# Kernel optimization log

Measured on AMD Instinct MI355X. Metric: run time of the kernel, lower is better.

Reference implementation:

```python
import jax, jax.numpy as jnp
import numpy as np

B, C, H, W = 8, 256, 128, 128
J = 8          # number of segmentation classes / fc_mu layers
S = 256        # style_length
EPS = 1e-5


def _conv3x3(x, w, b):
    # x: [B,S,H,W], w: [C,S,3,3] (OIHW), padding=1 -> SAME
    y = jax.lax.conv_general_dilated(
        x, w, window_strides=(1, 1), padding='SAME',
        dimension_numbers=('NCHW', 'OIHW', 'NCHW'))
    return y + b[None, :, None, None]


def setup_inputs() -> dict:
    key = jax.random.key(0)
    ks = jax.random.split(key, 12)
    fp = jax.random.normal(ks[0], (B, C, H, W), dtype=jnp.float32)
    # one-hot segmentation map (nearest-interpolated seg maps are one-hot)
    labels = jax.random.randint(ks[1], (B, H, W), 0, J)
    sg = jnp.transpose(jax.nn.one_hot(labels, J, dtype=jnp.float32), (0, 3, 1, 2))
    style_codes = jax.random.normal(ks[2], (B, J + 1, S), dtype=jnp.float32)
    mask_codes = jax.random.randint(ks[3], (B, J), 0, 2).astype(jnp.int32)
    # parameters
    bn_weight = jnp.ones((C,), jnp.float32)
    bn_bias = jnp.zeros((C,), jnp.float32)
    conv_gamma_w = jax.random.normal(ks[4], (C, S, 3, 3), jnp.float32) * 0.02
    conv_gamma_b = jnp.zeros((C,), jnp.float32)
    conv_beta_w = jax.random.normal(ks[5], (C, S, 3, 3), jnp.float32) * 0.02
    conv_beta_b = jnp.zeros((C,), jnp.float32)
    fc_w = jax.random.normal(ks[6], (J, S, S), jnp.float32) * 0.02  # [j, out, in]
    fc_b = jnp.zeros((J, S), jnp.float32)
    return dict(fp=fp, sg=sg, style_codes=style_codes, mask_codes=mask_codes,
                bn_weight=bn_weight, bn_bias=bn_bias,
                conv_gamma_w=conv_gamma_w, conv_gamma_b=conv_gamma_b,
                conv_beta_w=conv_beta_w, conv_beta_b=conv_beta_b,
                fc_w=fc_w, fc_b=fc_b)


def reference(fp, sg, style_codes, mask_codes, bn_weight, bn_bias,
              conv_gamma_w, conv_gamma_b, conv_beta_w, conv_beta_b,
              fc_w, fc_b):
    # BatchNorm2d (training-mode batch statistics, affine)
    mean = jnp.mean(fp, axis=(0, 2, 3), keepdims=True)
    var = jnp.var(fp, axis=(0, 2, 3), keepdims=True)
    xn = (fp - mean) * jax.lax.rsqrt(var + EPS)
    xn = xn * bn_weight[None, :, None, None] + bn_bias[None, :, None, None]

    nJ = sg.shape[1]
    # style code selection: j if mask_codes[b,j]==1 else nJ (the extra/shared code)
    idx = jnp.where(mask_codes == 1, jnp.arange(nJ)[None, :], nJ)        # [B,J]
    codes = jnp.take_along_axis(style_codes, idx[:, :, None], axis=1)    # [B,J,S]
    # per-region Linear (weights differ per region j) + ReLU
    mu = jax.nn.relu(jnp.einsum('bjs,jts->bjt', codes, fc_w) + fc_b[None])  # [B,J,S]
    # masked scatter of per-region style vectors (sg is one-hot -> exact)
    middle = jnp.einsum('bjhw,bjs->bshw', sg, mu)                         # [B,S,H,W]

    gamma = _conv3x3(middle, conv_gamma_w, conv_gamma_b)
    beta = _conv3x3(middle, conv_beta_w, conv_beta_b)
    return xn * (1.0 + gamma) + beta
```

## Files before the change

### kernel.cpp

```cpp
#include <hip/hip_runtime.h>
#include <hip/hip_fp16.h>
#include <stdint.h>

#define NB 8
#define NC 256
#define NH 128
#define NW 128
#define NJ 8
#define NS 256
#define NHW (NH*NW)
#define BN_EPS 1e-5f
#define TSTRIDE 68

__device__ inline __half2 u2h(uint32_t u) {
    union { uint32_t u; __half2 h; } x; x.u = u; return x.h;
}
__device__ inline uint32_t h2u(__half2 h) {
    union { uint32_t u; __half2 h; } x; x.h = h; return x.u;
}

__global__ __launch_bounds__(256) void kA(
        const float* __restrict__ fp, float* __restrict__ psum, float* __restrict__ psq,
        const float* __restrict__ sg, uint8_t* __restrict__ lab,
        const float* __restrict__ style, const int* __restrict__ mask,
        const float* __restrict__ fcw, const float* __restrict__ fcb,
        float* __restrict__ mu,
        const float* __restrict__ wg, const float* __restrict__ wb,
        float* __restrict__ wgt, float* __restrict__ wbt) {
    __shared__ float ls[4], lq[4];
    __shared__ float code[NS];
    __shared__ float tile[32][65];
    int blk = blockIdx.x;
    int t = threadIdx.x;
    if (blk < 2048) {
        int b = blk >> 8, c = blk & 255;
        const float4* p = (const float4*)(fp + (size_t)(b * NC + c) * NHW);
        float s = 0.f, q = 0.f;
        for (int i = t; i < NHW / 4; i += 256) {
            float4 v = p[i];
            s += v.x + v.y + v.z + v.w;
            q += v.x * v.x + v.y * v.y + v.z * v.z + v.w * v.w;
        }
        for (int o = 32; o > 0; o >>= 1) {
            s += __shfl_down(s, o);
            q += __shfl_down(q, o);
        }
        int wid = t >> 6, lane = t & 63;
        if (lane == 0) { ls[wid] = s; lq[wid] = q; }
        __syncthreads();
        if (t == 0) {
            float S2 = 0.f, Q2 = 0.f;
            for (int i = 0; i < 4; i++) { S2 += ls[i]; Q2 += lq[i]; }
            psum[c * 8 + b] = S2;
            psq[c * 8 + b] = Q2;
        }
    } else if (blk < 2560) {
        int pix = (blk - 2048) * 256 + t;
        int b = pix >> 14, hw = pix & 16383;
        const float* base = sg + (size_t)b * NJ * NHW + hw;
        int l = 0;
        #pragma unroll
        for (int j = 0; j < NJ; j++)
            if (base[(size_t)j * NHW] > 0.5f) l = j;
        lab[pix] = (uint8_t)l;
    } else if (blk < 2624) {
        int bj = blk - 2560;
        int b = bj >> 3, j = bj & 7;
        int row = (mask[bj] == 1) ? j : NJ;
        code[t] = style[((size_t)b * (NJ + 1) + row) * NS + t];
        __syncthreads();
        const float4* w4 = (const float4*)(fcw + ((size_t)j * NS + t) * NS);
        const float4* c4 = (const float4*)code;
        float acc = fcb[j * NS + t];
        for (int s4 = 0; s4 < NS / 4; s4++) {
            float4 wv = w4[s4];
            float4 cv = c4[s4];
            acc += wv.x * cv.x + wv.y * cv.y + wv.z * cv.z + wv.w * cv.w;
        }
        mu[bj * NS + t] = fmaxf(acc, 0.f);
    } else {
        int i = blk - 2624;
        int tb = i / 288, r = i - tb * 288;
        int skc = r % 72, cc = r / 72;
        int sk0 = skc * 32, c0 = cc * 64;
        const float* src = tb ? wb : wg;
        float* dst = tb ? wbt : wgt;
        {
            int skl = t & 31, cl = t >> 5;
            #pragma unroll
            for (int p = 0; p < 8; p++)
                tile[skl][cl + p * 8] = src[(size_t)(c0 + cl + p * 8) * 2304 + sk0 + skl];
        }
        __syncthreads();
        {
            int cl = t & 63, skl = t >> 6;
            #pragma unroll
            for (int p = 0; p < 8; p++) {
                int sk = sk0 + skl + p * 4;
                int s = sk / 9, k = sk - s * 9;
                dst[(size_t)k * (NS * NC) + (size_t)s * NC + c0 + cl] = tile[skl + p * 4][cl];
            }
        }
    }
}

__global__ __launch_bounds__(256) void kB(
        const float* __restrict__ psum, const float* __restrict__ psq,
        const float* __restrict__ bnw, const float* __restrict__ bnb,
        const float* __restrict__ cgb, const float* __restrict__ cbb,
        float2* __restrict__ Al, uint32_t* __restrict__ Bl,
        const float* __restrict__ mu, const float* __restrict__ wgt,
        const float* __restrict__ wbt, uint32_t* __restrict__ T) {
    int blk = blockIdx.x;
    int t = threadIdx.x;
    if (blk == 0) {
        int c = t;
        float s = 0.f, q = 0.f;
        for (int b = 0; b < NB; b++) { s += psum[c * 8 + b]; q += psq[c * 8 + b]; }
        const float N = (float)(NB * NHW);
        float mean = s / N;
        float var = q / N - mean * mean;
        if (var < 0.f) var = 0.f;
        float inv = 1.0f / sqrtf(var + BN_EPS);
        float a = bnw[c] * inv;
        float b2 = bnb[c] - mean * a;
        Al[c] = make_float2(a, b2);
        Bl[c] = h2u(__floats2half2_rn(1.0f + cgb[c], cbb[c]));
        return;
    }
    int bk = blk - 1;
    int b = bk / 9, k = bk - b * 9;
    __shared__ float m[NJ][NS];
    for (int i = t; i < NJ * NS; i += 256)
        ((float*)m)[i] = mu[(size_t)b * NJ * NS + i];
    __syncthreads();
    int c = t;
    float ag[NJ], ab[NJ];
    #pragma unroll
    for (int j = 0; j < NJ; j++) { ag[j] = 0.f; ab[j] = 0.f; }
    const float* pg = wgt + (size_t)k * NS * NC + c;
    const float* pb = wbt + (size_t)k * NS * NC + c;
    for (int s = 0; s < NS; s++) {
        float wgv = pg[(size_t)s * NC];
        float wbv = pb[(size_t)s * NC];
        #pragma unroll
        for (int j = 0; j < NJ; j++) {
            ag[j] += m[j][s] * wgv;
            ab[j] += m[j][s] * wbv;
        }
    }
    uint32_t* o = T + ((size_t)b * 9 + k) * 9 * NC + c;
    #pragma unroll
    for (int j = 0; j < NJ; j++)
        o[(size_t)j * NC] = h2u(__floats2half2_rn(ag[j], ab[j]));
    o[(size_t)8 * NC] = 0u;
}

__global__ __launch_bounds__(256, 5) void k_main(
        const float* __restrict__ fp, const uint8_t* __restrict__ lab,
        const uint32_t* __restrict__ T, const float2* __restrict__ Ag,
        const uint32_t* __restrict__ Bg, float* __restrict__ out) {
    int blk = blockIdx.x;
    int cc = blk & 3;
    int h  = (blk >> 2) & 127;
    int b  = blk >> 9;
    int c0 = cc * 64;

    __shared__ uint32_t Tl[81 * TSTRIDE];
    __shared__ float2   Apl[64];
    __shared__ uint32_t Bpl[64];
    __shared__ uint8_t  Ll[3][NW];

    int t = threadIdx.x;
    {
        const uint32_t* Tg = T + (size_t)b * 81 * NC + c0;
        int rr = t >> 4, ii = (t & 15) * 4;
        #pragma unroll
        for (int pass = 0; pass < 5; pass++) {
            int r = rr + pass * 16;
            *(uint4*)&Tl[r * TSTRIDE + ii] = *(const uint4*)&Tg[(size_t)r * NC + ii];
        }
        if (t < 16) *(uint4*)&Tl[80 * TSTRIDE + t * 4] = *(const uint4*)&Tg[(size_t)80 * NC + t * 4];
    }
    if (t < 64) { Apl[t] = Ag[c0 + t]; Bpl[t] = Bg[c0 + t]; }
    if (t >= 128 && t < 224) {
        int tt = t - 128;
        int r = tt >> 5, q = tt & 31;
        int hr = h - 1 + r;
        uint32_t v = 0;
        if (hr >= 0 && hr < NH)
            v = ((const uint32_t*)(lab + (size_t)b * NHW + (size_t)hr * NW))[q];
        ((uint32_t*)Ll)[tt] = v;
    }
    __syncthreads();

    int w = t & 127, cg = t >> 7;
    int base_k[9];
    #pragma unroll
    for (int dy = 0; dy < 3; dy++) {
        int hr = h - 1 + dy;
        bool rok = (hr >= 0) && (hr < NH);
        #pragma unroll
        for (int dx = 0; dx < 3; dx++) {
            int ww = w - 1 + dx;
            bool ok = rok && (ww >= 0) && (ww < NW);
            int wc = ww < 0 ? 0 : (ww > NW - 1 ? NW - 1 : ww);
            int j = ok ? (int)Ll[dy][wc] : 8;
            int k = dy * 3 + dx;
            base_k[k] = (k * 9 + j) * TSTRIDE + cg * 32;
        }
    }

    const float* fpb = fp + ((size_t)b * NC + c0 + cg * 32) * NHW + (size_t)h * NW + w;
    float*       ob  = out + ((size_t)b * NC + c0 + cg * 32) * NHW + (size_t)h * NW + w;

    #pragma unroll
    for (int q = 0; q < 8; q++) {
        uint4 bias = *(const uint4*)&Bpl[cg * 32 + q * 4];
        __half2 a0 = u2h(bias.x), a1 = u2h(bias.y), a2 = u2h(bias.z), a3 = u2h(bias.w);
        #pragma unroll
        for (int k = 0; k < 9; k++) {
            uint4 tv = *(const uint4*)&Tl[base_k[k] + q * 4];
            a0 = __hadd2(a0, u2h(tv.x));
            a1 = __hadd2(a1, u2h(tv.y));
            a2 = __hadd2(a2, u2h(tv.z));
            a3 = __hadd2(a3, u2h(tv.w));
        }
        float4 ap01 = *(const float4*)&Apl[cg * 32 + q * 4];
        float4 ap23 = *(const float4*)&Apl[cg * 32 + q * 4 + 2];
        float x0 = fpb[(size_t)(q * 4 + 0) * NHW];
        float x1 = fpb[(size_t)(q * 4 + 1) * NHW];
        float x2 = fpb[(size_t)(q * 4 + 2) * NHW];
        float x3 = fpb[(size_t)(q * 4 + 3) * NHW];
        float2 g0 = __half22float2(a0);
        float2 g1 = __half22float2(a1);
        float2 g2 = __half22float2(a2);
        float2 g3 = __half22float2(a3);
        __builtin_nontemporal_store((x0 * ap01.x + ap01.y) * g0.x + g0.y, &ob[(size_t)(q * 4 + 0) * NHW]);
        __builtin_nontemporal_store((x1 * ap01.z + ap01.w) * g1.x + g1.y, &ob[(size_t)(q * 4 + 1) * NHW]);
        __builtin_nontemporal_store((x2 * ap23.x + ap23.y) * g2.x + g2.y, &ob[(size_t)(q * 4 + 2) * NHW]);
        __builtin_nontemporal_store((x3 * ap23.z + ap23.w) * g3.x + g3.y, &ob[(size_t)(q * 4 + 3) * NHW]);
    }
}

extern "C" void kernel_launch(void* const* d_in, const int* in_sizes, int n_in,
                              void* d_out, int out_size, void* d_ws, size_t ws_size,
                              hipStream_t stream) {
    const float* fp    = (const float*)d_in[0];
    const float* sg    = (const float*)d_in[1];
    const float* style = (const float*)d_in[2];
    const int*   mask  = (const int*)d_in[3];
    const float* bnw   = (const float*)d_in[4];
    const float* bnb   = (const float*)d_in[5];
    const float* cgw   = (const float*)d_in[6];
    const float* cgb   = (const float*)d_in[7];
    const float* cbw   = (const float*)d_in[8];
    const float* cbb   = (const float*)d_in[9];
    const float* fcw   = (const float*)d_in[10];
    const float* fcb   = (const float*)d_in[11];
    float* out = (float*)d_out;

    char* ws = (char*)d_ws;
    float*    psum = (float*)(ws + 0);
    float*    psq  = (float*)(ws + 8192);
    float2*   Al   = (float2*)(ws + 16384);
    uint32_t* Bl   = (uint32_t*)(ws + 18432);
    uint8_t*  lab  = (uint8_t*)(ws + 19456);
    float*    mu   = (float*)(ws + 150528);
    float*    wgt  = (float*)(ws + 216064);
    float*    wbt  = (float*)(ws + 2575360);
    uint32_t* T    = (uint32_t*)(ws + 4934656);

    hipLaunchKernelGGL(kA, dim3(3200), dim3(256), 0, stream,
                       fp, psum, psq, sg, lab, style, mask, fcw, fcb, mu,
                       cgw, cbw, wgt, wbt);
    hipLaunchKernelGGL(kB, dim3(73), dim3(256), 0, stream,
                       psum, psq, bnw, bnb, cgb, cbb, Al, Bl, mu, wgt, wbt, T);
    hipLaunchKernelGGL(k_main, dim3(NB * NH * 4), dim3(256), 0, stream,
                       fp, lab, T, Al, Bl, out);
}
```

Before: 104.0 us.

## Pack gamma/beta conv weights into half2 and widen kB to 1024 threads

The weight-transpose stage now reads both the gamma and beta conv weights in one block, using nontemporal loads, and writes a single packed half2 array instead of two fp32 arrays. This halves the intermediate weight traffic written by kA and read by kB. kB now runs 1024 threads per block, with each thread handling two of the eight classes, and keeps mu transposed in shared memory, so per-thread register use drops and more parallelism is exposed. Weights are rounded to fp16 before the style-projection accumulation rather than only at output, which adds some rounding error.

```diff
diff --git a/kernel.cpp b/kernel.cpp
--- a/kernel.cpp
+++ b/kernel.cpp
@@ -26,10 +26,10 @@
         const float* __restrict__ fcw, const float* __restrict__ fcb,
         float* __restrict__ mu,
         const float* __restrict__ wg, const float* __restrict__ wb,
-        float* __restrict__ wgt, float* __restrict__ wbt) {
+        uint32_t* __restrict__ wpk) {
     __shared__ float ls[4], lq[4];
     __shared__ float code[NS];
-    __shared__ float tile[32][65];
+    __shared__ uint32_t tileu[32][65];
     int blk = blockIdx.x;
     int t = threadIdx.x;
     if (blk < 2048) {
@@ -80,16 +80,17 @@
         mu[bj * NS + t] = fmaxf(acc, 0.f);
     } else {
         int i = blk - 2624;
-        int tb = i / 288, r = i - tb * 288;
-        int skc = r % 72, cc = r / 72;
+        int skc = i % 72, cc = i / 72;
         int sk0 = skc * 32, c0 = cc * 64;
-        const float* src = tb ? wb : wg;
-        float* dst = tb ? wbt : wgt;
         {
             int skl = t & 31, cl = t >> 5;
             #pragma unroll
-            for (int p = 0; p < 8; p++)
-                tile[skl][cl + p * 8] = src[(size_t)(c0 + cl + p * 8) * 2304 + sk0 + skl];
+            for (int p = 0; p < 8; p++) {
+                int c = c0 + cl + p * 8;
+                float g  = __builtin_nontemporal_load(&wg[(size_t)c * 2304 + sk0 + skl]);
+                float b2 = __builtin_nontemporal_load(&wb[(size_t)c * 2304 + sk0 + skl]);
+                tileu[skl][cl + p * 8] = h2u(__floats2half2_rn(g, b2));
+            }
         }
         __syncthreads();
         {
@@ -98,62 +99,59 @@
             for (int p = 0; p < 8; p++) {
                 int sk = sk0 + skl + p * 4;
                 int s = sk / 9, k = sk - s * 9;
-                dst[(size_t)k * (NS * NC) + (size_t)s * NC + c0 + cl] = tile[skl + p * 4][cl];
+                wpk[(size_t)k * (NS * NC) + (size_t)s * NC + c0 + cl] = tileu[skl + p * 4][cl];
             }
         }
     }
 }
 
-__global__ __launch_bounds__(256) void kB(
+__global__ __launch_bounds__(1024) void kB(
         const float* __restrict__ psum, const float* __restrict__ psq,
         const float* __restrict__ bnw, const float* __restrict__ bnb,
         const float* __restrict__ cgb, const float* __restrict__ cbb,
         float2* __restrict__ Al, uint32_t* __restrict__ Bl,
-        const float* __restrict__ mu, const float* __restrict__ wgt,
-        const float* __restrict__ wbt, uint32_t* __restrict__ T) {
+        const float* __restrict__ mu, const uint32_t* __restrict__ wpk,
+        uint32_t* __restrict__ T) {
     int blk = blockIdx.x;
     int t = threadIdx.x;
-    if (blk == 0) {
-        int c = t;
-        float s = 0.f, q = 0.f;
-        for (int b = 0; b < NB; b++) { s += psum[c * 8 + b]; q += psq[c * 8 + b]; }
-        const float N = (float)(NB * NHW);
-        float mean = s / N;
-        float var = q / N - mean * mean;
-        if (var < 0.f) var = 0.f;
-        float inv = 1.0f / sqrtf(var + BN_EPS);
-        float a = bnw[c] * inv;
-        float b2 = bnb[c] - mean * a;
-        Al[c] = make_float2(a, b2);
-        Bl[c] = h2u(__floats2half2_rn(1.0f + cgb[c], cbb[c]));
+    if (blk == 72) {
+        if (t < 256) {
+            int c = t;
+            float s = 0.f, q = 0.f;
+            for (int b = 0; b < NB; b++) { s += psum[c * 8 + b]; q += psq[c * 8 + b]; }
+            const float N = (float)(NB * NHW);
+            float mean = s / N;
+            float var = q / N - mean * mean;
+            if (var < 0.f) var = 0.f;
+            float inv = 1.0f / sqrtf(var + BN_EPS);
+            float a = bnw[c] * inv;
+            float b2 = bnb[c] - mean * a;
+            Al[c] = make_float2(a, b2);
+            Bl[c] = h2u(__floats2half2_rn(1.0f + cgb[c], cbb[c]));
+        }
         return;
     }
-    int bk = blk - 1;
-    int b = bk / 9, k = bk - b * 9;
-    __shared__ float m[NJ][NS];
-    for (int i = t; i < NJ * NS; i += 256)
-        ((float*)m)[i] = mu[(size_t)b * NJ * NS + i];
+    int b = blk / 9, k = blk - b * 9;
+    __shared__ float ms[NS * NJ];
+    for (int i = t; i < NJ * NS; i += 1024) {
+        int j = i >> 8, s = i & 255;
+        ms[s * 8 + j] = mu[(size_t)b * NJ * NS + i];
+    }
     __syncthreads();
-    int c = t;
-    float ag[NJ], ab[NJ];
-    #pragma unroll
-    for (int j = 0; j < NJ; j++) { ag[j] = 0.f; ab[j] = 0.f; }
-    const float* pg = wgt + (size_t)k * NS * NC + c;
-    const float* pb = wbt + (size_t)k * NS * NC + c;
+    int c = t & 255, jq = t >> 8;
+    int j0 = jq * 2;
+    const uint32_t* wp = wpk + (size_t)k * NS * NC + c;
+    float g0 = 0.f, be0 = 0.f, g1 = 0.f, be1 = 0.f;
     for (int s = 0; s < NS; s++) {
-        float wgv = pg[(size_t)s * NC];
-        float wbv = pb[(size_t)s * NC];
-        #pragma unroll
-        for (int j = 0; j < NJ; j++) {
-            ag[j] += m[j][s] * wgv;
-            ab[j] += m[j][s] * wbv;
-        }
+        float2 w2 = __half22float2(u2h(wp[(size_t)s * NC]));
+        float2 mm = *(const float2*)&ms[s * 8 + j0];
+        g0  += mm.x * w2.x;  be0 += mm.x * w2.y;
+        g1  += mm.y * w2.x;  be1 += mm.y * w2.y;
     }
     uint32_t* o = T + ((size_t)b * 9 + k) * 9 * NC + c;
-    #pragma unroll
-    for (int j = 0; j < NJ; j++)
-        o[(size_t)j * NC] = h2u(__floats2half2_rn(ag[j], ab[j]));
-    o[(size_t)8 * NC] = 0u;
+    o[(size_t)j0 * NC]       = h2u(__floats2half2_rn(g0, be0));
+    o[(size_t)(j0 + 1) * NC] = h2u(__floats2half2_rn(g1, be1));
+    if (jq == 0) o[(size_t)8 * NC] = 0u;
 }
 
 __global__ __launch_bounds__(256, 5) void k_main(
@@ -267,15 +265,14 @@
     uint32_t* Bl   = (uint32_t*)(ws + 18432);
     uint8_t*  lab  = (uint8_t*)(ws + 19456);
     float*    mu   = (float*)(ws + 150528);
-    float*    wgt  = (float*)(ws + 216064);
-    float*    wbt  = (float*)(ws + 2575360);
-    uint32_t* T    = (uint32_t*)(ws + 4934656);
-
-    hipLaunchKernelGGL(kA, dim3(3200), dim3(256), 0, stream,
+    uint32_t* wpk  = (uint32_t*)(ws + 216064);
+    uint32_t* T    = (uint32_t*)(ws + 2575360);
+
+    hipLaunchKernelGGL(kA, dim3(2912), dim3(256), 0, stream,
                        fp, psum, psq, sg, lab, style, mask, fcw, fcb, mu,
-                       cgw, cbw, wgt, wbt);
-    hipLaunchKernelGGL(kB, dim3(73), dim3(256), 0, stream,
-                       psum, psq, bnw, bnb, cgb, cbb, Al, Bl, mu, wgt, wbt, T);
+                       cgw, cbw, wpk);
+    hipLaunchKernelGGL(kB, dim3(73), dim3(1024), 0, stream,
+                       psum, psq, bnw, bnb, cgb, cbb, Al, Bl, mu, wpk, T);
     hipLaunchKernelGGL(k_main, dim3(NB * NH * 4), dim3(256), 0, stream,
                        fp, lab, T, Al, Bl, out);
 }
```

After: 90.54 us. 1.15x faster.
